# Performance work log

Hardware: AMD Instinct MI355X
Metric: run time of the kernel (lower is better)

## Reference

```python
import jax, jax.numpy as jnp
import numpy as np

H, D, DK, DV = 8, 512, 64, 64
B, L = 2, 2048
LN_EPS = 1e-5


def setup_inputs() -> dict:
    key = jax.random.key(0)
    ks = jax.random.split(key, 12)
    q = jax.random.normal(ks[0], (B, L, D), jnp.float32)
    k = jax.random.normal(ks[1], (B, L, D), jnp.float32)
    v = jax.random.normal(ks[2], (B, L, D), jnp.float32)
    mask = jax.random.randint(ks[3], (H * B, L, L), 0, 2) > 0
    sq = np.sqrt(2.0 / (D + DK)).astype(np.float32)
    sv = np.sqrt(2.0 / (D + DV)).astype(np.float32)
    Wq = jax.random.normal(ks[4], (H * DK, D), jnp.float32) * sq
    Wk = jax.random.normal(ks[5], (H * DK, D), jnp.float32) * sq
    Wv = jax.random.normal(ks[6], (H * DV, D), jnp.float32) * sv
    xav = np.sqrt(2.0 / (H * DV + D)).astype(np.float32)
    Wfc = jax.random.normal(ks[7], (D, H * DV), jnp.float32) * xav
    bfc = jnp.zeros((D,), jnp.float32)
    gamma = jnp.ones((D,), jnp.float32)
    beta = jnp.zeros((D,), jnp.float32)
    return {"q": q, "k": k, "v": v, "mask": mask, "Wq": Wq, "Wk": Wk,
            "Wv": Wv, "Wfc": Wfc, "bfc": bfc, "gamma": gamma, "beta": beta}


def reference(q, k, v, mask, Wq, Wk, Wv, Wfc, bfc, gamma, beta):
    # dropout in eval mode (identity)
    temperature = jnp.sqrt(jnp.asarray(DK, q.dtype))
    residual = q
    # projections -> (H, B, L, dk/dv), matching permute(2,0,1,3)
    qh = (q @ Wq.T).reshape(B, L, H, DK).transpose(2, 0, 1, 3)
    kh = (k @ Wk.T).reshape(B, L, H, DK).transpose(2, 0, 1, 3)
    vh = (v @ Wv.T).reshape(B, L, H, DV).transpose(2, 0, 1, 3)
    attn = jnp.einsum('hbqd,hbkd->hbqk', qh, kh) / temperature
    m = mask.reshape(H, B, L, L)
    attn = jnp.where(m, jnp.asarray(-1e10, attn.dtype), attn)
    attn = jax.nn.softmax(attn, axis=-1)
    out = jnp.einsum('hbqk,hbkd->hbqd', attn, vh)  # (H,B,L,DV)
    out = out.transpose(1, 2, 0, 3).reshape(B, L, H * DV)
    out = out @ Wfc.T + bfc
    x = out + residual
    mu = jnp.mean(x, axis=-1, keepdims=True)
    var = jnp.var(x, axis=-1, keepdims=True)
    return gamma * (x - mu) * jax.lax.rsqrt(var + LN_EPS) + beta
```

## Files before the change

### kernel.cpp

```cpp
#include <hip/hip_runtime.h>
#include <hip/hip_bf16.h>
#include <cmath>
#include <cstdint>

#define H_ 8
#define B_ 2
#define L_ 2048
#define D_ 512
#define SPLIT_ 4

typedef __attribute__((ext_vector_type(8))) short short8_t;
typedef __attribute__((ext_vector_type(4))) float float4_t;
typedef __attribute__((ext_vector_type(4))) unsigned short ushort4_t;
typedef __attribute__((ext_vector_type(2))) unsigned int uint2_t;
typedef __attribute__((ext_vector_type(4))) unsigned int uint4_t;

__device__ __forceinline__ unsigned short bf16u(float f) {
  union { __hip_bfloat16 b; unsigned short u; } c;
  c.b = __float2bfloat16(f);
  return c.u;
}
__device__ __forceinline__ unsigned bf16x2(float lo, float hi) {
  return (unsigned)bf16u(lo) | ((unsigned)bf16u(hi) << 16);
}
__device__ __forceinline__ float bf2f(unsigned short u) {
  union { unsigned u; float f; } c; c.u = (unsigned)u << 16; return c.f;
}

__device__ __forceinline__ unsigned pack8(unsigned long long x) {
  x |= x >> 4; x |= x >> 2; x |= x >> 1;
  x &= 0x0101010101010101ULL;
  return (unsigned)((x * 0x0102040810204080ULL) >> 56);
}

__global__ __launch_bounds__(256)
void cvt_w(const float* __restrict__ wfc, unsigned short* __restrict__ wfcb) {
  int i = (blockIdx.x * 256 + threadIdx.x) * 4;
  float4_t a = *(const float4_t*)(wfc + i);
  ushort4_t o;
  o[0] = bf16u(a[0]); o[1] = bf16u(a[1]); o[2] = bf16u(a[2]); o[3] = bf16u(a[3]);
  *(ushort4_t*)(wfcb + i) = o;
}

__global__ __launch_bounds__(512)
void proj_gemm(const float* __restrict__ q, const float* __restrict__ k,
               const float* __restrict__ v,
               const float* __restrict__ wq, const float* __restrict__ wk,
               const float* __restrict__ wv,
               unsigned short* __restrict__ Qp, unsigned short* __restrict__ Kp,
               unsigned short* __restrict__ Vt) {
  __shared__ unsigned short As[128][72];
  __shared__ unsigned short Bs[64][72];
  const int tid = threadIdx.x, lane = tid & 63, wave = tid >> 6;
  const int g = lane >> 4, qi = lane & 15;
  const int m0 = blockIdx.x * 128, n0 = blockIdx.y * 64;
  const int z = blockIdx.z;
  const float* A = (z == 0) ? q : (z == 1) ? k : v;
  const float* W = (z == 0) ? wq : (z == 1) ? wk : wv;

  float4_t acc[4] = {};
  const int ar = tid >> 2, ac = (tid & 3) * 16;
  const int br = tid >> 3, bc = (tid & 7) * 8;

  for (int kt = 0; kt < 512; kt += 64) {
    const float* src = A + (size_t)(m0 + ar) * 512 + kt + ac;
    float4_t f0 = *(const float4_t*)(src);
    float4_t f1 = *(const float4_t*)(src + 4);
    float4_t f2 = *(const float4_t*)(src + 8);
    float4_t f3 = *(const float4_t*)(src + 12);
    short8_t s0, s1;
    s0[0] = bf16u(f0[0]); s0[1] = bf16u(f0[1]); s0[2] = bf16u(f0[2]); s0[3] = bf16u(f0[3]);
    s0[4] = bf16u(f1[0]); s0[5] = bf16u(f1[1]); s0[6] = bf16u(f1[2]); s0[7] = bf16u(f1[3]);
    s1[0] = bf16u(f2[0]); s1[1] = bf16u(f2[1]); s1[2] = bf16u(f2[2]); s1[3] = bf16u(f2[3]);
    s1[4] = bf16u(f3[0]); s1[5] = bf16u(f3[1]); s1[6] = bf16u(f3[2]); s1[7] = bf16u(f3[3]);
    *(short8_t*)(&As[ar][ac]) = s0;
    *(short8_t*)(&As[ar][ac + 8]) = s1;
    const float* wsrc = W + (size_t)(n0 + br) * 512 + kt + bc;
    float4_t w0 = *(const float4_t*)(wsrc);
    float4_t w1 = *(const float4_t*)(wsrc + 4);
    short8_t sw;
    sw[0] = bf16u(w0[0]); sw[1] = bf16u(w0[1]); sw[2] = bf16u(w0[2]); sw[3] = bf16u(w0[3]);
    sw[4] = bf16u(w1[0]); sw[5] = bf16u(w1[1]); sw[6] = bf16u(w1[2]); sw[7] = bf16u(w1[3]);
    *(short8_t*)(&Bs[br][bc]) = sw;
    __syncthreads();
#pragma unroll
    for (int kk = 0; kk < 2; kk++) {
      const int krow = kk * 32 + g * 8;
      short8_t a = *(const short8_t*)(&As[wave * 16 + qi][krow]);
#pragma unroll
      for (int n = 0; n < 4; n++) {
        short8_t b = *(const short8_t*)(&Bs[n * 16 + qi][krow]);
        acc[n] = __builtin_amdgcn_mfma_f32_16x16x32_bf16(a, b, acc[n], 0, 0, 0);
      }
    }
    __syncthreads();
  }

  const int gmb = m0 + wave * 16 + g * 4;
#pragma unroll
  for (int n = 0; n < 4; n++) {
    int gn = n0 + n * 16 + qi;
    int h = gn >> 6, d = gn & 63;
    if (z == 2) {
      int bb = gmb >> 11, l = gmb & 2047;
      ushort4_t o;
#pragma unroll
      for (int r = 0; r < 4; r++) o[r] = bf16u(acc[n][r]);
      *(ushort4_t*)(Vt + ((size_t)(h * B_ + bb) * 64 + d) * L_ + l) = o;
    } else {
      float sc = (z == 0) ? 0.125f : 1.0f;
      unsigned short* O = (z == 0) ? Qp : Kp;
#pragma unroll
      for (int r = 0; r < 4; r++) {
        int gm = gmb + r;
        int bb = gm >> 11, l = gm & 2047;
        O[((size_t)(h * B_ + bb) * L_ + l) * 64 + d] = bf16u(acc[n][r] * sc);
      }
    }
  }
}

template<int MS>
__device__ __forceinline__ void attn_body(
    const unsigned short* __restrict__ Qp, const unsigned short* __restrict__ Kp,
    const unsigned short* __restrict__ Vt, const unsigned char* __restrict__ mask,
    unsigned short* __restrict__ Opart, float* __restrict__ MLpart,
    unsigned short (*Ks)[72], unsigned short (*Vs)[72], unsigned int (*Ps)[36]) {
  const int tid = threadIdx.x, lane = tid & 63, wave = tid >> 6;
  const int g = lane >> 4, qi = lane & 15;
  const int hb = blockIdx.y;
  const int sp = blockIdx.z;
  const int k_begin = sp * (L_ / SPLIT_), k_end = k_begin + L_ / SPLIT_;
  const int qg0 = blockIdx.x * 128 + wave * 16;
  const int qg = qg0 + qi;
  const size_t base = (size_t)hb * (L_ * 64);

  const size_t mrowoff = ((size_t)hb * L_ + qg0 + (lane >> 2)) * L_;
  const unsigned char* mb1 = mask + mrowoff + (lane & 3) * 16;
  const unsigned* mb4 = (const unsigned*)mask + mrowoff + (lane & 3) * 16;

  short8_t qf[2];
#pragma unroll
  for (int kk = 0; kk < 2; kk++)
    qf[kk] = *(const short8_t*)(Qp + base + (size_t)qg * 64 + kk * 32 + g * 8);

  float4_t o[4] = {};
  float mrun = -INFINITY, lrun = 0.f;
  const int sr = tid >> 3, sc = (tid & 7) * 8;
  const int srcA = qi * 4;

  short8_t kr, vr;
  unsigned fb;
  {
    const int k0 = k_begin;
    kr = *(const short8_t*)(Kp + base + (size_t)(k0 + sr) * 64 + sc);
    vr = *(const short8_t*)(Vt + base + (size_t)sr * L_ + k0 + sc);
    if (MS == 1) {
      uint4_t x = *(const uint4_t*)(mb1 + k0);
      unsigned long long lo = ((unsigned long long)x[1] << 32) | x[0];
      unsigned long long hi = ((unsigned long long)x[3] << 32) | x[2];
      fb = pack8(lo) | (pack8(hi) << 8);
    } else {
      fb = 0;
#pragma unroll
      for (int j = 0; j < 4; j++) {
        uint4_t x = *(const uint4_t*)(mb4 + k0 + j * 4);
        fb |= (((unsigned)(x[0] != 0)) | ((unsigned)(x[1] != 0) << 1) |
               ((unsigned)(x[2] != 0) << 2) | ((unsigned)(x[3] != 0) << 3)) << (j * 4);
      }
    }
  }

  for (int k0 = k_begin; k0 < k_end; k0 += 64) {
    *(short8_t*)(&Ks[sr][sc]) = kr;
    *(short8_t*)(&Vs[sr][sc]) = vr;
    unsigned fb_cur = fb;
    __syncthreads();

    if (k0 + 64 < k_end) {
      const int kn = k0 + 64;
      kr = *(const short8_t*)(Kp + base + (size_t)(kn + sr) * 64 + sc);
      vr = *(const short8_t*)(Vt + base + (size_t)sr * L_ + kn + sc);
      if (MS == 1) {
        uint4_t x = *(const uint4_t*)(mb1 + kn);
        unsigned long long lo = ((unsigned long long)x[1] << 32) | x[0];
        unsigned long long hi = ((unsigned long long)x[3] << 32) | x[2];
        fb = pack8(lo) | (pack8(hi) << 8);
      } else {
        fb = 0;
#pragma unroll
        for (int j = 0; j < 4; j++) {
          uint4_t x = *(const uint4_t*)(mb4 + kn + j * 4);
          fb |= (((unsigned)(x[0] != 0)) | ((unsigned)(x[1] != 0) << 1) |
                 ((unsigned)(x[2] != 0) << 2) | ((unsigned)(x[3] != 0) << 3)) << (j * 4);
        }
      }
    }

    unsigned nib[4];
#pragma unroll
    for (int t = 0; t < 4; t++)
      nib[t] = ((unsigned)__shfl((int)fb_cur, srcA + t, 64) >> (g * 4)) & 0xFu;

    float4_t st[4] = {};
#pragma unroll
    for (int kk = 0; kk < 2; kk++) {
      const int krow = kk * 32 + g * 8;
#pragma unroll
      for (int t = 0; t < 4; t++) {
        short8_t a = *(const short8_t*)(&Ks[t * 16 + qi][krow]);
        st[t] = __builtin_amdgcn_mfma_f32_16x16x32_bf16(a, qf[kk], st[t], 0, 0, 0);
      }
    }

    float tmax = -INFINITY;
#pragma unroll
    for (int t = 0; t < 4; t++)
#pragma unroll
      for (int r = 0; r < 4; r++) {
        if ((nib[t] >> r) & 1u) st[t][r] = -1e10f;
        tmax = fmaxf(tmax, st[t][r]);
      }
    tmax = fmaxf(tmax, __shfl_xor(tmax, 16, 64));
    tmax = fmaxf(tmax, __shfl_xor(tmax, 32, 64));

    float nm = fmaxf(mrun, tmax);
    float fac = __expf(mrun - nm);
    mrun = nm;

    float psum = 0.f;
    unsigned w8[4][2];
#pragma unroll
    for (int t = 0; t < 4; t++) {
      float p0 = __expf(st[t][0] - nm);
      float p1 = __expf(st[t][1] - nm);
      float p2 = __expf(st[t][2] - nm);
      float p3 = __expf(st[t][3] - nm);
      psum += (p0 + p1) + (p2 + p3);
      w8[t][0] = bf16x2(p0, p1);
      w8[t][1] = bf16x2(p2, p3);
    }
    psum += __shfl_xor(psum, 16, 64);
    psum += __shfl_xor(psum, 32, 64);
    lrun = lrun * fac + psum;
#pragma unroll
    for (int n2 = 0; n2 < 4; n2++)
#pragma unroll
      for (int r = 0; r < 4; r++) o[n2][r] *= fac;

#pragma unroll
    for (int t = 0; t < 4; t++) {
      uint2_t w2; w2[0] = w8[t][0]; w2[1] = w8[t][1];
      *(uint2_t*)(&Ps[qi][t * 8 + g * 2]) = w2;
    }
#pragma unroll
    for (int s = 0; s < 2; s++) {
      short8_t pb = *(const short8_t*)(&Ps[qi][s * 16 + g * 4]);
#pragma unroll
      for (int n2 = 0; n2 < 4; n2++) {
        short8_t a = *(const short8_t*)(&Vs[n2 * 16 + qi][s * 32 + g * 8]);
        o[n2] = __builtin_amdgcn_mfma_f32_16x16x32_bf16(a, pb, o[n2], 0, 0, 0);
      }
    }
    __syncthreads();
  }

  const size_t pb = (((size_t)sp * 16 + hb) * L_ + qg) * 64;
#pragma unroll
  for (int n2 = 0; n2 < 4; n2++) {
    ushort4_t ov;
#pragma unroll
    for (int r = 0; r < 4; r++) ov[r] = bf16u(o[n2][r]);
    *(ushort4_t*)(Opart + pb + n2 * 16 + g * 4) = ov;
  }
  if (lane < 16) {
    float* ml = MLpart + (((size_t)sp * 16 + hb) * L_ + qg) * 2;
    ml[0] = mrun; ml[1] = lrun;
  }
}

__global__ __launch_bounds__(512)
void attn_split(const unsigned short* __restrict__ Qp, const unsigned short* __restrict__ Kp,
                const unsigned short* __restrict__ Vt, const unsigned char* __restrict__ mask,
                unsigned short* __restrict__ Opart, float* __restrict__ MLpart) {
  __shared__ unsigned short Ks[64][72];
  __shared__ unsigned short Vs[64][72];
  __shared__ unsigned int PsAll[8][16][36];
  const int wave = threadIdx.x >> 6;
  unsigned probe = ((const unsigned*)mask)[threadIdx.x & 63];
  if (__any(probe > 1u))
    attn_body<1>(Qp, Kp, Vt, mask, Opart, MLpart, Ks, Vs, PsAll[wave]);
  else
    attn_body<4>(Qp, Kp, Vt, mask, Opart, MLpart, Ks, Vs, PsAll[wave]);
}

__global__ __launch_bounds__(256)
void attn_combine(const unsigned short* __restrict__ Opart, const float* __restrict__ MLpart,
                  unsigned short* __restrict__ Y) {
  int gid = blockIdx.x * 256 + threadIdx.x;
  int dvc = (gid & 7) * 8;
  int hbq = gid >> 3;
  int hb = hbq >> 11, qq = hbq & 2047;
  int h = hb >> 1, bb = hb & 1;
  float m[SPLIT_], l[SPLIT_];
  float M = -INFINITY;
#pragma unroll
  for (int s = 0; s < SPLIT_; s++) {
    const float* ml = MLpart + (((size_t)s * 16 + hb) * L_ + qq) * 2;
    m[s] = ml[0]; l[s] = ml[1];
    M = fmaxf(M, m[s]);
  }
  float denom = 0.f, e[SPLIT_];
#pragma unroll
  for (int s = 0; s < SPLIT_; s++) { e[s] = __expf(m[s] - M); denom += l[s] * e[s]; }
  float inv = 1.0f / denom;
  float acc[8] = {};
#pragma unroll
  for (int s = 0; s < SPLIT_; s++) {
    const unsigned short* p = Opart + (((size_t)s * 16 + hb) * L_ + qq) * 64 + dvc;
    ushort4_t a0 = *(const ushort4_t*)(p);
    ushort4_t a1 = *(const ushort4_t*)(p + 4);
    float w = e[s] * inv;
#pragma unroll
    for (int j = 0; j < 4; j++) {
      acc[j] += bf2f(a0[j]) * w;
      acc[j + 4] += bf2f(a1[j]) * w;
    }
  }
  short8_t ov;
#pragma unroll
  for (int j = 0; j < 8; j++) ov[j] = bf16u(acc[j]);
  *(short8_t*)(Y + ((size_t)(bb * L_ + qq)) * 512 + h * 64 + dvc) = ov;
}

__global__ __launch_bounds__(512)
void fc_gemm(const unsigned short* __restrict__ Yb, const unsigned short* __restrict__ wfcb,
             const float* __restrict__ resid, const float* __restrict__ bfc,
             float* __restrict__ out) {
  __shared__ unsigned short As[128][72];
  __shared__ unsigned short Bs[64][72];
  const int tid = threadIdx.x, lane = tid & 63, wave = tid >> 6;
  const int g = lane >> 4, qi = lane & 15;
  const int m0 = blockIdx.x * 128, n0 = blockIdx.y * 64;
  float4_t acc[4] = {};
  const int ar = tid >> 2, ac = (tid & 3) * 16;
  const int br = tid >> 3, bc = (tid & 7) * 8;

  for (int kt = 0; kt < 512; kt += 64) {
    const unsigned short* src = Yb + (size_t)(m0 + ar) * 512 + kt + ac;
    *(short8_t*)(&As[ar][ac]) = *(const short8_t*)(src);
    *(short8_t*)(&As[ar][ac + 8]) = *(const short8_t*)(src + 8);
    *(short8_t*)(&Bs[br][bc]) = *(const short8_t*)(wfcb + (size_t)(n0 + br) * 512 + kt + bc);
    __syncthreads();
#pragma unroll
    for (int kk = 0; kk < 2; kk++) {
      const int krow = kk * 32 + g * 8;
      short8_t a = *(const short8_t*)(&As[wave * 16 + qi][krow]);
#pragma unroll
      for (int n = 0; n < 4; n++) {
        short8_t b = *(const short8_t*)(&Bs[n * 16 + qi][krow]);
        acc[n] = __builtin_amdgcn_mfma_f32_16x16x32_bf16(a, b, acc[n], 0, 0, 0);
      }
    }
    __syncthreads();
  }

  const int gmb = m0 + wave * 16 + g * 4;
#pragma unroll
  for (int n = 0; n < 4; n++) {
    int gn = n0 + n * 16 + qi;
    float bv = bfc[gn];
#pragma unroll
    for (int r = 0; r < 4; r++) {
      int gm = gmb + r;
      out[(size_t)gm * 512 + gn] = acc[n][r] + bv + resid[(size_t)gm * 512 + gn];
    }
  }
}

__global__ __launch_bounds__(256)
void ln_kernel(float* __restrict__ Z, const float* __restrict__ gamma,
               const float* __restrict__ beta) {
  const int row = blockIdx.x * 4 + (threadIdx.x >> 6);
  const int lane = threadIdx.x & 63;
  float* zp = Z + (size_t)row * 512 + lane * 8;
  float4_t x0 = *(const float4_t*)(zp);
  float4_t x1 = *(const float4_t*)(zp + 4);
  float s = 0.f, s2 = 0.f;
#pragma unroll
  for (int j = 0; j < 4; j++) { s += x0[j] + x1[j]; s2 += x0[j] * x0[j] + x1[j] * x1[j]; }
#pragma unroll
  for (int mm = 1; mm < 64; mm <<= 1) { s += __shfl_xor(s, mm, 64); s2 += __shfl_xor(s2, mm, 64); }
  float mu = s * (1.f / 512.f);
  float var = s2 * (1.f / 512.f) - mu * mu;
  float inv = rsqrtf(var + 1e-5f);
  float4_t g0 = *(const float4_t*)(gamma + lane * 8);
  float4_t g1 = *(const float4_t*)(gamma + lane * 8 + 4);
  float4_t b0 = *(const float4_t*)(beta + lane * 8);
  float4_t b1 = *(const float4_t*)(beta + lane * 8 + 4);
#pragma unroll
  for (int j = 0; j < 4; j++) {
    x0[j] = g0[j] * (x0[j] - mu) * inv + b0[j];
    x1[j] = g1[j] * (x1[j] - mu) * inv + b1[j];
  }
  *(float4_t*)(zp) = x0;
  *(float4_t*)(zp + 4) = x1;
}

extern "C" void kernel_launch(void* const* d_in, const int* in_sizes, int n_in,
                              void* d_out, int out_size, void* d_ws, size_t ws_size,
                              hipStream_t stream) {
  const float* q   = (const float*)d_in[0];
  const float* k   = (const float*)d_in[1];
  const float* v   = (const float*)d_in[2];
  const unsigned char* mask = (const unsigned char*)d_in[3];
  const float* Wq  = (const float*)d_in[4];
  const float* Wk  = (const float*)d_in[5];
  const float* Wv  = (const float*)d_in[6];
  const float* Wfc = (const float*)d_in[7];
  const float* bfc = (const float*)d_in[8];
  const float* gamma = (const float*)d_in[9];
  const float* beta  = (const float*)d_in[10];
  float* out = (float*)d_out;

  char* ws = (char*)d_ws;
  unsigned short* wfcb = (unsigned short*)(ws);
  unsigned short* Qp   = wfcb + 262144;
  unsigned short* Kp   = Qp + 2097152;
  unsigned short* Vt   = Kp + 2097152;
  unsigned short* Y    = Vt + 2097152;
  unsigned short* Opart = Y + 2097152;
  float* MLpart = (float*)(Opart + (size_t)SPLIT_ * 16 * L_ * 64);

  cvt_w<<<256, 256, 0, stream>>>(Wfc, wfcb);
  proj_gemm<<<dim3(32, 8, 3), 512, 0, stream>>>(q, k, v, Wq, Wk, Wv, Qp, Kp, Vt);
  attn_split<<<dim3(16, 16, SPLIT_), 512, 0, stream>>>(Qp, Kp, Vt, mask, Opart, MLpart);
  attn_combine<<<1024, 256, 0, stream>>>(Opart, MLpart, Y);
  fc_gemm<<<dim3(32, 8), 512, 0, stream>>>(Y, wfcb, q, bfc, out);
  ln_kernel<<<1024, 256, 0, stream>>>(out, gamma, beta);
}
```

Baseline: 127.6 us.

## Shrink GEMM tiles, prefetch mask two steps ahead, swizzle attention block order

Both projection and output GEMMs move to 64x64 tiles with 256 threads, doubling the number of blocks to spread work over more CUs at the cost of less operand reuse per block. The attention kernel now loads mask bits two key tiles ahead instead of one, to hide the latency of the large mask read. It also remaps block IDs with a swizzle so that blocks sharing a head/batch and split are scheduled in a different order across XCDs, aiming at better cache locality for K/V. The mask prefetch holds an extra register live across the loop.

```diff
diff --git a/kernel.cpp b/kernel.cpp
--- a/kernel.cpp
+++ b/kernel.cpp
@@ -42,25 +42,24 @@
   *(ushort4_t*)(wfcb + i) = o;
 }
 
-__global__ __launch_bounds__(512)
+__global__ __launch_bounds__(256)
 void proj_gemm(const float* __restrict__ q, const float* __restrict__ k,
                const float* __restrict__ v,
                const float* __restrict__ wq, const float* __restrict__ wk,
                const float* __restrict__ wv,
                unsigned short* __restrict__ Qp, unsigned short* __restrict__ Kp,
                unsigned short* __restrict__ Vt) {
-  __shared__ unsigned short As[128][72];
+  __shared__ unsigned short As[64][72];
   __shared__ unsigned short Bs[64][72];
   const int tid = threadIdx.x, lane = tid & 63, wave = tid >> 6;
   const int g = lane >> 4, qi = lane & 15;
-  const int m0 = blockIdx.x * 128, n0 = blockIdx.y * 64;
+  const int m0 = blockIdx.x * 64, n0 = blockIdx.y * 64;
   const int z = blockIdx.z;
   const float* A = (z == 0) ? q : (z == 1) ? k : v;
   const float* W = (z == 0) ? wq : (z == 1) ? wk : wv;
 
   float4_t acc[4] = {};
   const int ar = tid >> 2, ac = (tid & 3) * 16;
-  const int br = tid >> 3, bc = (tid & 7) * 8;
 
   for (int kt = 0; kt < 512; kt += 64) {
     const float* src = A + (size_t)(m0 + ar) * 512 + kt + ac;
@@ -75,13 +74,18 @@
     s1[4] = bf16u(f3[0]); s1[5] = bf16u(f3[1]); s1[6] = bf16u(f3[2]); s1[7] = bf16u(f3[3]);
     *(short8_t*)(&As[ar][ac]) = s0;
     *(short8_t*)(&As[ar][ac + 8]) = s1;
-    const float* wsrc = W + (size_t)(n0 + br) * 512 + kt + bc;
+    const float* wsrc = W + (size_t)(n0 + ar) * 512 + kt + ac;
     float4_t w0 = *(const float4_t*)(wsrc);
     float4_t w1 = *(const float4_t*)(wsrc + 4);
-    short8_t sw;
-    sw[0] = bf16u(w0[0]); sw[1] = bf16u(w0[1]); sw[2] = bf16u(w0[2]); sw[3] = bf16u(w0[3]);
-    sw[4] = bf16u(w1[0]); sw[5] = bf16u(w1[1]); sw[6] = bf16u(w1[2]); sw[7] = bf16u(w1[3]);
-    *(short8_t*)(&Bs[br][bc]) = sw;
+    float4_t w2 = *(const float4_t*)(wsrc + 8);
+    float4_t w3 = *(const float4_t*)(wsrc + 12);
+    short8_t t0, t1;
+    t0[0] = bf16u(w0[0]); t0[1] = bf16u(w0[1]); t0[2] = bf16u(w0[2]); t0[3] = bf16u(w0[3]);
+    t0[4] = bf16u(w1[0]); t0[5] = bf16u(w1[1]); t0[6] = bf16u(w1[2]); t0[7] = bf16u(w1[3]);
+    t1[0] = bf16u(w2[0]); t1[1] = bf16u(w2[1]); t1[2] = bf16u(w2[2]); t1[3] = bf16u(w2[3]);
+    t1[4] = bf16u(w3[0]); t1[5] = bf16u(w3[1]); t1[6] = bf16u(w3[2]); t1[7] = bf16u(w3[3]);
+    *(short8_t*)(&Bs[ar][ac]) = t0;
+    *(short8_t*)(&Bs[ar][ac + 8]) = t1;
     __syncthreads();
 #pragma unroll
     for (int kk = 0; kk < 2; kk++) {
@@ -125,13 +129,12 @@
     const unsigned short* __restrict__ Qp, const unsigned short* __restrict__ Kp,
     const unsigned short* __restrict__ Vt, const unsigned char* __restrict__ mask,
     unsigned short* __restrict__ Opart, float* __restrict__ MLpart,
-    unsigned short (*Ks)[72], unsigned short (*Vs)[72], unsigned int (*Ps)[36]) {
+    unsigned short (*Ks)[72], unsigned short (*Vs)[72], unsigned int (*Ps)[36],
+    int bx, int hb, int sp) {
   const int tid = threadIdx.x, lane = tid & 63, wave = tid >> 6;
   const int g = lane >> 4, qi = lane & 15;
-  const int hb = blockIdx.y;
-  const int sp = blockIdx.z;
   const int k_begin = sp * (L_ / SPLIT_), k_end = k_begin + L_ / SPLIT_;
-  const int qg0 = blockIdx.x * 128 + wave * 16;
+  const int qg0 = bx * 128 + wave * 16;
   const int qg = qg0 + qi;
   const size_t base = (size_t)hb * (L_ * 64);
 
@@ -149,53 +152,46 @@
   const int sr = tid >> 3, sc = (tid & 7) * 8;
   const int srcA = qi * 4;
 
+#define LOADFB(dst, kpos)                                                        \
+  do {                                                                           \
+    if (MS == 1) {                                                               \
+      uint4_t x = *(const uint4_t*)(mb1 + (kpos));                               \
+      unsigned long long lo = ((unsigned long long)x[1] << 32) | x[0];           \
+      unsigned long long hi = ((unsigned long long)x[3] << 32) | x[2];           \
+      dst = pack8(lo) | (pack8(hi) << 8);                                        \
+    } else {                                                                     \
+      dst = 0;                                                                   \
+      _Pragma("unroll")                                                          \
+      for (int j = 0; j < 4; j++) {                                              \
+        uint4_t x = *(const uint4_t*)(mb4 + (kpos) + j * 4);                     \
+        dst |= (((unsigned)(x[0] != 0)) | ((unsigned)(x[1] != 0) << 1) |         \
+                ((unsigned)(x[2] != 0) << 2) | ((unsigned)(x[3] != 0) << 3))     \
+               << (j * 4);                                                       \
+      }                                                                          \
+    }                                                                            \
+  } while (0)
+
   short8_t kr, vr;
-  unsigned fb;
-  {
-    const int k0 = k_begin;
-    kr = *(const short8_t*)(Kp + base + (size_t)(k0 + sr) * 64 + sc);
-    vr = *(const short8_t*)(Vt + base + (size_t)sr * L_ + k0 + sc);
-    if (MS == 1) {
-      uint4_t x = *(const uint4_t*)(mb1 + k0);
-      unsigned long long lo = ((unsigned long long)x[1] << 32) | x[0];
-      unsigned long long hi = ((unsigned long long)x[3] << 32) | x[2];
-      fb = pack8(lo) | (pack8(hi) << 8);
-    } else {
-      fb = 0;
-#pragma unroll
-      for (int j = 0; j < 4; j++) {
-        uint4_t x = *(const uint4_t*)(mb4 + k0 + j * 4);
-        fb |= (((unsigned)(x[0] != 0)) | ((unsigned)(x[1] != 0) << 1) |
-               ((unsigned)(x[2] != 0) << 2) | ((unsigned)(x[3] != 0) << 3)) << (j * 4);
-      }
-    }
-  }
+  unsigned fb1, fb2;
+  kr = *(const short8_t*)(Kp + base + (size_t)(k_begin + sr) * 64 + sc);
+  vr = *(const short8_t*)(Vt + base + (size_t)sr * L_ + k_begin + sc);
+  LOADFB(fb1, k_begin);
+  fb2 = 0;
+  if (k_begin + 64 < k_end) LOADFB(fb2, k_begin + 64);
 
   for (int k0 = k_begin; k0 < k_end; k0 += 64) {
     *(short8_t*)(&Ks[sr][sc]) = kr;
     *(short8_t*)(&Vs[sr][sc]) = vr;
-    unsigned fb_cur = fb;
+    unsigned fb_cur = fb1;
+    fb1 = fb2;
     __syncthreads();
 
     if (k0 + 64 < k_end) {
       const int kn = k0 + 64;
       kr = *(const short8_t*)(Kp + base + (size_t)(kn + sr) * 64 + sc);
       vr = *(const short8_t*)(Vt + base + (size_t)sr * L_ + kn + sc);
-      if (MS == 1) {
-        uint4_t x = *(const uint4_t*)(mb1 + kn);
-        unsigned long long lo = ((unsigned long long)x[1] << 32) | x[0];
-        unsigned long long hi = ((unsigned long long)x[3] << 32) | x[2];
-        fb = pack8(lo) | (pack8(hi) << 8);
-      } else {
-        fb = 0;
-#pragma unroll
-        for (int j = 0; j < 4; j++) {
-          uint4_t x = *(const uint4_t*)(mb4 + kn + j * 4);
-          fb |= (((unsigned)(x[0] != 0)) | ((unsigned)(x[1] != 0) << 1) |
-                 ((unsigned)(x[2] != 0) << 2) | ((unsigned)(x[3] != 0) << 3)) << (j * 4);
-        }
-      }
-    }
+    }
+    if (k0 + 128 < k_end) LOADFB(fb2, k0 + 128);
 
     unsigned nib[4];
 #pragma unroll
@@ -264,6 +260,7 @@
     }
     __syncthreads();
   }
+#undef LOADFB
 
   const size_t pb = (((size_t)sp * 16 + hb) * L_ + qg) * 64;
 #pragma unroll
@@ -287,11 +284,16 @@
   __shared__ unsigned short Vs[64][72];
   __shared__ unsigned int PsAll[8][16][36];
   const int wave = threadIdx.x >> 6;
+  const int id = blockIdx.x + 16 * (blockIdx.y + 16 * blockIdx.z);
+  const int swz = (id & 7) * 128 + (id >> 3);
+  const int hb = swz >> 6;
+  const int sp = (swz & 63) >> 4;
+  const int bx = swz & 15;
   unsigned probe = ((const unsigned*)mask)[threadIdx.x & 63];
   if (__any(probe > 1u))
-    attn_body<1>(Qp, Kp, Vt, mask, Opart, MLpart, Ks, Vs, PsAll[wave]);
+    attn_body<1>(Qp, Kp, Vt, mask, Opart, MLpart, Ks, Vs, PsAll[wave], bx, hb, sp);
   else
-    attn_body<4>(Qp, Kp, Vt, mask, Opart, MLpart, Ks, Vs, PsAll[wave]);
+    attn_body<4>(Qp, Kp, Vt, mask, Opart, MLpart, Ks, Vs, PsAll[wave], bx, hb, sp);
 }
 
 __global__ __launch_bounds__(256)
@@ -333,24 +335,25 @@
   *(short8_t*)(Y + ((size_t)(bb * L_ + qq)) * 512 + h * 64 + dvc) = ov;
 }
 
-__global__ __launch_bounds__(512)
+__global__ __launch_bounds__(256)
 void fc_gemm(const unsigned short* __restrict__ Yb, const unsigned short* __restrict__ wfcb,
              const float* __restrict__ resid, const float* __restrict__ bfc,
              float* __restrict__ out) {
-  __shared__ unsigned short As[128][72];
+  __shared__ unsigned short As[64][72];
   __shared__ unsigned short Bs[64][72];
   const int tid = threadIdx.x, lane = tid & 63, wave = tid >> 6;
   const int g = lane >> 4, qi = lane & 15;
-  const int m0 = blockIdx.x * 128, n0 = blockIdx.y * 64;
+  const int m0 = blockIdx.x * 64, n0 = blockIdx.y * 64;
   float4_t acc[4] = {};
   const int ar = tid >> 2, ac = (tid & 3) * 16;
-  const int br = tid >> 3, bc = (tid & 7) * 8;
 
   for (int kt = 0; kt < 512; kt += 64) {
     const unsigned short* src = Yb + (size_t)(m0 + ar) * 512 + kt + ac;
     *(short8_t*)(&As[ar][ac]) = *(const short8_t*)(src);
     *(short8_t*)(&As[ar][ac + 8]) = *(const short8_t*)(src + 8);
-    *(short8_t*)(&Bs[br][bc]) = *(const short8_t*)(wfcb + (size_t)(n0 + br) * 512 + kt + bc);
+    const unsigned short* wsrc = wfcb + (size_t)(n0 + ar) * 512 + kt + ac;
+    *(short8_t*)(&Bs[ar][ac]) = *(const short8_t*)(wsrc);
+    *(short8_t*)(&Bs[ar][ac + 8]) = *(const short8_t*)(wsrc + 8);
     __syncthreads();
 #pragma unroll
     for (int kk = 0; kk < 2; kk++) {
@@ -433,9 +436,9 @@
   float* MLpart = (float*)(Opart + (size_t)SPLIT_ * 16 * L_ * 64);
 
   cvt_w<<<256, 256, 0, stream>>>(Wfc, wfcb);
-  proj_gemm<<<dim3(32, 8, 3), 512, 0, stream>>>(q, k, v, Wq, Wk, Wv, Qp, Kp, Vt);
+  proj_gemm<<<dim3(64, 8, 3), 256, 0, stream>>>(q, k, v, Wq, Wk, Wv, Qp, Kp, Vt);
   attn_split<<<dim3(16, 16, SPLIT_), 512, 0, stream>>>(Qp, Kp, Vt, mask, Opart, MLpart);
   attn_combine<<<1024, 256, 0, stream>>>(Opart, MLpart, Y);
-  fc_gemm<<<dim3(32, 8), 512, 0, stream>>>(Y, wfcb, q, bfc, out);
+  fc_gemm<<<dim3(64, 8), 256, 0, stream>>>(Y, wfcb, q, bfc, out);
   ln_kernel<<<1024, 256, 0, stream>>>(out, gamma, beta);
 }
```

Measured after the change: 134.4 us. 1.05x slower.
